# Kernel optimization log

Hardware: AMD Instinct MI355X
Metric: run time of the kernel (lower is better)

Reference implementation:

```python
import jax, jax.numpy as jnp
import numpy as np

B, S, E, H = 2, 2048, 1024, 16
D = E // H  # head_dim = 64


def setup_inputs() -> dict:
    key = jax.random.key(0)
    ks = jax.random.split(key, 6)
    sc = 0.02
    return {
        "hidden_states": jax.random.normal(ks[0], (B, S, E), dtype=jnp.float32),
        "attn_bias": jax.random.normal(ks[1], (S, S), dtype=jnp.float32) * sc,
        "Wqkv": jax.random.normal(ks[2], (E, 3 * E), dtype=jnp.float32) * sc,
        "bqkv": jax.random.normal(ks[3], (3 * E,), dtype=jnp.float32) * sc,
        "Wproj": jax.random.normal(ks[4], (E, E), dtype=jnp.float32) * sc,
        "bproj": jax.random.normal(ks[5], (E,), dtype=jnp.float32) * sc,
    }


def reference(hidden_states, attn_bias, Wqkv, bqkv, Wproj, bproj):
    b, s, e = hidden_states.shape
    qkv = hidden_states @ Wqkv + bqkv                      # [b,s,3e]
    q, k, v = jnp.split(qkv, 3, axis=-1)                   # each [b,s,e]
    cache_key, cache_value = k, v                          # kvCache
    # [b,h,s,d]
    qh = q.reshape(b, s, H, D).transpose(0, 2, 1, 3)
    kh = k.reshape(b, s, H, D).transpose(0, 2, 1, 3)
    vh = v.reshape(b, s, H, D).transpose(0, 2, 1, 3)
    scores = jnp.einsum("bhqd,bhkd->bhqk", qh, kh) / jnp.sqrt(jnp.float32(D))
    scores = scores + attn_bias[:s, :s][None, None]        # learned additive bias
    causal = jnp.tril(jnp.ones((s, s), dtype=bool))
    scores = jnp.where(causal[None, None], scores, jnp.float32(-1e9))
    attn = jax.nn.softmax(scores, axis=-1)
    ctx = jnp.einsum("bhqk,bhkd->bhqd", attn, vh)
    ctx = ctx.transpose(0, 2, 1, 3).reshape(b, s, e)
    out = ctx @ Wproj + bproj                              # resid dropout p=0 -> identity
    return (out, cache_key, cache_value)
```

## Files before the change

### kernel.cpp

```cpp
#include <hip/hip_runtime.h>

#define B_ 2
#define S_ 2048
#define E_ 1024
#define H_ 16
#define D_ 64

typedef short  s16x8 __attribute__((ext_vector_type(8)));
typedef float  f32x4 __attribute__((ext_vector_type(4)));
typedef unsigned short u16x4 __attribute__((ext_vector_type(4)));

__device__ __forceinline__ ushort f2bf(float f) {
    union { float f; unsigned u; } x; x.f = f;
    unsigned u = x.u + 0x7fffu + ((x.u >> 16) & 1u);
    return (ushort)(u >> 16);
}

__global__ __launch_bounds__(256) void cvtx_kernel(
    const float* __restrict__ X, ushort* __restrict__ Xbf)
{
    int i = (blockIdx.x * 256 + threadIdx.x) * 4;
    float4 v = *(const float4*)&X[i];
    u16x4 o;
    o.x = f2bf(v.x); o.y = f2bf(v.y); o.z = f2bf(v.z); o.w = f2bf(v.w);
    *(u16x4*)&Xbf[i] = o;
}

__global__ __launch_bounds__(256) void wtrans_kernel(
    const float* __restrict__ W, ushort* __restrict__ Wt, int Kdim, int Ndim)
{
    __shared__ float tile[64][65];
    int n0 = blockIdx.x * 64, k0 = blockIdx.y * 64;
    int tid = threadIdx.x;
    int c = tid & 63;
#pragma unroll
    for (int r = tid >> 6; r < 64; r += 4)
        tile[r][c] = W[(size_t)(k0 + r) * Ndim + n0 + c];
    __syncthreads();
#pragma unroll
    for (int r = tid >> 6; r < 64; r += 4)
        Wt[(size_t)(n0 + r) * Kdim + k0 + c] = f2bf(tile[c][r]);
}

__global__ __launch_bounds__(256) void gemm_mfma_bt(
    const ushort* __restrict__ A,
    const ushort* __restrict__ Bt,
    const float* __restrict__ bias,
    int M, int N, int K,
    float* __restrict__ C0,
    ushort* __restrict__ Qbf, float* __restrict__ Kf32, ushort* __restrict__ Kbf,
    float* __restrict__ Vf32, int mode)
{
    __shared__ ushort As[128 * 32];
    __shared__ ushort Bs[128 * 32];
    int tid = threadIdx.x;
    int wid = tid >> 6, lane = tid & 63;
    int l15 = lane & 15, quad = lane >> 4;
    int wm = wid >> 1, wn = wid & 1;
    int row0 = blockIdx.y * 128, col0 = blockIdx.x * 128;

    int sr = wid * 16 + (lane >> 2);
    int sk = (lane & 3) * 8;

    f32x4 acc[4][4];
#pragma unroll
    for (int mt = 0; mt < 4; mt++)
#pragma unroll
        for (int nt = 0; nt < 4; nt++) acc[mt][nt] = (f32x4){0.f, 0.f, 0.f, 0.f};

    for (int k0 = 0; k0 < K; k0 += 32) {
        __syncthreads();
#pragma unroll
        for (int c = 0; c < 2; c++) {
            int r = c * 64 + sr;
            __builtin_amdgcn_global_load_lds(
                (const __attribute__((address_space(1))) unsigned int*)
                    &A[(size_t)(row0 + r) * K + k0 + sk],
                (__attribute__((address_space(3))) unsigned int*)&As[r * 32 + sk],
                16, 0, 0);
            __builtin_amdgcn_global_load_lds(
                (const __attribute__((address_space(1))) unsigned int*)
                    &Bt[(size_t)(col0 + r) * K + k0 + sk],
                (__attribute__((address_space(3))) unsigned int*)&Bs[r * 32 + sk],
                16, 0, 0);
        }
        __syncthreads();

        s16x8 af[4], bf[4];
#pragma unroll
        for (int mt = 0; mt < 4; mt++)
            af[mt] = *(const s16x8*)&As[(wm * 64 + mt * 16 + l15) * 32 + quad * 8];
#pragma unroll
        for (int nt = 0; nt < 4; nt++)
            bf[nt] = *(const s16x8*)&Bs[(wn * 64 + nt * 16 + l15) * 32 + quad * 8];
#pragma unroll
        for (int mt = 0; mt < 4; mt++)
#pragma unroll
            for (int nt = 0; nt < 4; nt++)
                acc[mt][nt] = __builtin_amdgcn_mfma_f32_16x16x32_bf16(
                    af[mt], bf[nt], acc[mt][nt], 0, 0, 0);
    }

#pragma unroll
    for (int nt = 0; nt < 4; nt++) {
        int n = col0 + wn * 64 + nt * 16 + l15;
        float bv = bias[n];
        if (mode == 1) {
            int seg = n >> 10;
            int nn = n & (E_ - 1);
#pragma unroll
            for (int mt = 0; mt < 4; mt++)
#pragma unroll
                for (int r = 0; r < 4; r++) {
                    int row = row0 + wm * 64 + mt * 16 + quad * 4 + r;
                    float v = acc[mt][nt][r] + bv;
                    size_t idx = (size_t)row * E_ + nn;
                    if (seg == 0)      Qbf[idx] = f2bf(v);
                    else if (seg == 1) { Kf32[idx] = v; Kbf[idx] = f2bf(v); }
                    else               Vf32[idx] = v;
                }
        } else {
#pragma unroll
            for (int mt = 0; mt < 4; mt++)
#pragma unroll
                for (int r = 0; r < 4; r++) {
                    int row = row0 + wm * 64 + mt * 16 + quad * 4 + r;
                    C0[(size_t)row * N + n] = acc[mt][nt][r] + bv;
                }
        }
    }
}

__global__ __launch_bounds__(256) void vtrans_kernel(
    const float* __restrict__ V, ushort* __restrict__ Vt)
{
    __shared__ float tile[64][65];
    int blk = blockIdx.x;
    int s0 = (blk & 31) * 64;
    int bh = blk >> 5;
    int b = bh >> 4, h = bh & 15;
    int tid = threadIdx.x;
    int d = tid & 63;
#pragma unroll
    for (int i = tid >> 6; i < 64; i += 4)
        tile[i][d] = V[((size_t)(b * S_ + s0 + i)) * E_ + h * 64 + d];
    __syncthreads();
    int lane = tid & 63, w = tid >> 6;
#pragma unroll
    for (int dd = w; dd < 64; dd += 4)
        Vt[((size_t)(bh * 64 + dd)) * S_ + s0 + lane] = f2bf(tile[lane][dd]);
}

__global__ __launch_bounds__(256) void attn_mfma_kernel(
    const ushort* __restrict__ Qbf,
    const ushort* __restrict__ Kbf,
    const ushort* __restrict__ Vt,
    const float* __restrict__ bias,
    ushort* __restrict__ Ctx)
{
    __shared__ ushort Ks[64][72];
    __shared__ ushort Vs[64][72];
    __shared__ ushort Ps[4][16][72];

    int blk = blockIdx.x;
    int bh = blk & 31;
    int pr = blk >> 5;
    int b = bh >> 4, h = bh & 15;
    int tid = threadIdx.x;
    int wid = tid >> 6, lane = tid & 63;
    int l15 = lane & 15, quad = lane >> 4;

    int skey = tid >> 2;
    int scol = (tid & 3) * 16;
    const float scale = 0.125f;

    const size_t krow = (size_t)(b * S_ + skey) * E_ + h * 64 + scol;
    const size_t vrow = (size_t)(bh * 64 + skey) * S_ + scol;

    for (int half = 0; half < 2; half++) {
        int qt = half ? pr : (31 - pr);
        int q0w = qt * 64 + wid * 16;

        const size_t qbase = ((size_t)(b * S_ + q0w + l15)) * E_ + h * 64 + quad * 8;
        s16x8 qa0 = *(const s16x8*)&Qbf[qbase];
        s16x8 qa1 = *(const s16x8*)&Qbf[qbase + 32];

        f32x4 o[4];
#pragma unroll
        for (int dt = 0; dt < 4; dt++) o[dt] = (f32x4){0.f, 0.f, 0.f, 0.f};
        float lsum[4];
#pragma unroll
        for (int r = 0; r < 4; r++) lsum[r] = 0.f;

        float4 kr0 = ((const float4*)&Kbf[krow])[0];
        float4 kr1 = ((const float4*)&Kbf[krow])[1];
        float4 vr0 = ((const float4*)&Vt[vrow])[0];
        float4 vr1 = ((const float4*)&Vt[vrow])[1];
        float bvn[4][4];
#pragma unroll
        for (int r = 0; r < 4; r++)
#pragma unroll
            for (int kt = 0; kt < 4; kt++)
                bvn[r][kt] = bias[(size_t)(q0w + quad * 4 + r) * S_ + kt * 16 + l15];

        for (int t = 0; t <= qt; t++) {
            int j0 = t * 64;
            __syncthreads();
            *(float4*)&Ks[skey][scol]     = kr0;
            *(float4*)&Ks[skey][scol + 8] = kr1;
            *(float4*)&Vs[skey][scol]     = vr0;
            *(float4*)&Vs[skey][scol + 8] = vr1;
            float bv[4][4];
#pragma unroll
            for (int r = 0; r < 4; r++)
#pragma unroll
                for (int kt = 0; kt < 4; kt++) bv[r][kt] = bvn[r][kt];
            __syncthreads();

            if (t < qt) {
                int j1 = j0 + 64;
                kr0 = ((const float4*)&Kbf[krow + (size_t)j1 * E_])[0];
                kr1 = ((const float4*)&Kbf[krow + (size_t)j1 * E_])[1];
                vr0 = ((const float4*)&Vt[vrow + j1])[0];
                vr1 = ((const float4*)&Vt[vrow + j1])[1];
#pragma unroll
                for (int r = 0; r < 4; r++)
#pragma unroll
                    for (int kt = 0; kt < 4; kt++)
                        bvn[r][kt] = bias[(size_t)(q0w + quad * 4 + r) * S_ + j1 + kt * 16 + l15];
            }

            f32x4 s[4];
#pragma unroll
            for (int kt = 0; kt < 4; kt++) {
                s16x8 kb0 = *(const s16x8*)&Ks[kt * 16 + l15][quad * 8];
                s16x8 kb1 = *(const s16x8*)&Ks[kt * 16 + l15][quad * 8 + 32];
                f32x4 acc = (f32x4){0.f, 0.f, 0.f, 0.f};
                acc = __builtin_amdgcn_mfma_f32_16x16x32_bf16(qa0, kb0, acc, 0, 0, 0);
                acc = __builtin_amdgcn_mfma_f32_16x16x32_bf16(qa1, kb1, acc, 0, 0, 0);
                s[kt] = acc;
            }

            bool diag = (t == qt);
#pragma unroll
            for (int r = 0; r < 4; r++) {
                int row = q0w + quad * 4 + r;
#pragma unroll
                for (int kt = 0; kt < 4; kt++) {
                    int j = j0 + kt * 16 + l15;
                    float v = s[kt][r] * scale + bv[r][kt];
                    float p = (diag && j > row) ? 0.f : __expf(v);
                    lsum[r] += p;
                    int chunk = (kt * 2 + (l15 >> 3)) ^ quad;
                    Ps[wid][quad * 4 + r][chunk * 8 + (l15 & 7)] = f2bf(p);
                }
            }

            int cb = (quad ^ (l15 >> 2)) * 8;
            s16x8 pa0 = *(const s16x8*)&Ps[wid][l15][cb];
            s16x8 pa1 = *(const s16x8*)&Ps[wid][l15][cb + 32];
#pragma unroll
            for (int dt = 0; dt < 4; dt++) {
                s16x8 vb0 = *(const s16x8*)&Vs[dt * 16 + l15][quad * 8];
                s16x8 vb1 = *(const s16x8*)&Vs[dt * 16 + l15][quad * 8 + 32];
                o[dt] = __builtin_amdgcn_mfma_f32_16x16x32_bf16(pa0, vb0, o[dt], 0, 0, 0);
                o[dt] = __builtin_amdgcn_mfma_f32_16x16x32_bf16(pa1, vb1, o[dt], 0, 0, 0);
            }
        }

        float inv_l[4];
#pragma unroll
        for (int r = 0; r < 4; r++) {
            float l = lsum[r];
            l += __shfl_xor(l, 1);
            l += __shfl_xor(l, 2);
            l += __shfl_xor(l, 4);
            l += __shfl_xor(l, 8);
            inv_l[r] = 1.f / l;
        }

#pragma unroll
        for (int dt = 0; dt < 4; dt++) {
#pragma unroll
            for (int r = 0; r < 4; r++) {
                int row = q0w + quad * 4 + r;
                Ctx[((size_t)(b * S_ + row)) * E_ + h * 64 + dt * 16 + l15] =
                    f2bf(o[dt][r] * inv_l[r]);
            }
        }
    }
}

extern "C" void kernel_launch(void* const* d_in, const int* in_sizes, int n_in,
                              void* d_out, int out_size, void* d_ws, size_t ws_size,
                              hipStream_t stream) {
    const float* X     = (const float*)d_in[0];
    const float* abias = (const float*)d_in[1];
    const float* Wqkv  = (const float*)d_in[2];
    const float* bqkv  = (const float*)d_in[3];
    const float* Wproj = (const float*)d_in[4];
    const float* bproj = (const float*)d_in[5];

    const size_t plane = (size_t)B_ * S_ * E_;
    float* out  = (float*)d_out;
    float* kout = out + plane;
    float* vout = kout + plane;

    ushort* xbf    = (ushort*)d_ws;
    ushort* qbf    = xbf + plane;
    ushort* kbf    = qbf + plane;
    ushort* vt     = kbf + plane;
    ushort* ctxbf  = xbf;
    ushort* wqkvt  = vt + plane;
    ushort* wprojt = wqkvt + (size_t)3 * E_ * E_;

    const int M = B_ * S_;

    cvtx_kernel<<<dim3(plane / 1024), 256, 0, stream>>>(X, xbf);
    wtrans_kernel<<<dim3(3 * E_ / 64, E_ / 64), 256, 0, stream>>>(Wqkv, wqkvt, E_, 3 * E_);
    wtrans_kernel<<<dim3(E_ / 64, E_ / 64), 256, 0, stream>>>(Wproj, wprojt, E_, E_);

    gemm_mfma_bt<<<dim3(3 * E_ / 128, M / 128), 256, 0, stream>>>(
        xbf, wqkvt, bqkv, M, 3 * E_, E_,
        nullptr, qbf, kout, kbf, vout, 1);

    vtrans_kernel<<<dim3(B_ * H_ * (S_ / 64)), 256, 0, stream>>>(vout, vt);

    attn_mfma_kernel<<<dim3(B_ * H_ * 16), 256, 0, stream>>>(
        qbf, kbf, vt, abias, ctxbf);

    gemm_mfma_bt<<<dim3(E_ / 128, M / 128), 256, 0, stream>>>(
        ctxbf, wprojt, bproj, M, E_, E_,
        out, nullptr, nullptr, nullptr, nullptr, 0);
}
```

Before: 235.2 us.

## Split attention key loop across two wave groups per query slice

Doubles the attention block to 512 threads. Two waves now share each 16-row query slice and handle alternating 64-key tiles, with K/V staged in two LDS buffers. Partial outputs and row sums are combined through shared memory at the end. The goal is more parallelism and latency hiding, since the grid has only 512 blocks. The cost is extra LDS traffic, an extra reduction step and higher register pressure under the 512-thread bound.

Result: slower. 258.0 us (+9.7%).

```diff
diff --git a/kernel.cpp b/kernel.cpp
--- a/kernel.cpp
+++ b/kernel.cpp
@@ -151,16 +151,18 @@
         Vt[((size_t)(bh * 64 + dd)) * S_ + s0 + lane] = f2bf(tile[lane][dd]);
 }
 
-__global__ __launch_bounds__(256) void attn_mfma_kernel(
+__global__ __launch_bounds__(512, 4) void attn_mfma_kernel(
     const ushort* __restrict__ Qbf,
     const ushort* __restrict__ Kbf,
     const ushort* __restrict__ Vt,
     const float* __restrict__ bias,
     ushort* __restrict__ Ctx)
 {
-    __shared__ ushort Ks[64][72];
-    __shared__ ushort Vs[64][72];
-    __shared__ ushort Ps[4][16][72];
+    __shared__ ushort Ks[2][64][72];
+    __shared__ ushort Vs[2][64][72];
+    __shared__ ushort Ps[8][16][72];
+    f32x4 (*Om)[4][64]   = (f32x4(*)[4][64])Ps;
+    float (*Lm)[2][64][4] = (float(*)[2][64][4])Ks;
 
     int blk = blockIdx.x;
     int bh = blk & 31;
@@ -169,9 +171,13 @@
     int tid = threadIdx.x;
     int wid = tid >> 6, lane = tid & 63;
     int l15 = lane & 15, quad = lane >> 4;
-
-    int skey = tid >> 2;
-    int scol = (tid & 3) * 16;
+    int qslice = wid >> 1;
+    int par = wid & 1;
+
+    int ts = tid & 255;
+    int par_s = tid >> 8;
+    int skey = ts >> 2;
+    int scol = (ts & 3) * 16;
     const float scale = 0.125f;
 
     const size_t krow = (size_t)(b * S_ + skey) * E_ + h * 64 + scol;
@@ -179,7 +185,8 @@
 
     for (int half = 0; half < 2; half++) {
         int qt = half ? pr : (31 - pr);
-        int q0w = qt * 64 + wid * 16;
+        int q0w = qt * 64 + qslice * 16;
+        int U = (qt + 2) >> 1;
 
         const size_t qbase = ((size_t)(b * S_ + q0w + l15)) * E_ + h * 64 + quad * 8;
         s16x8 qa0 = *(const s16x8*)&Qbf[qbase];
@@ -192,24 +199,35 @@
 #pragma unroll
         for (int r = 0; r < 4; r++) lsum[r] = 0.f;
 
-        float4 kr0 = ((const float4*)&Kbf[krow])[0];
-        float4 kr1 = ((const float4*)&Kbf[krow])[1];
-        float4 vr0 = ((const float4*)&Vt[vrow])[0];
-        float4 vr1 = ((const float4*)&Vt[vrow])[1];
+        int t0 = (par_s <= qt) ? par_s : qt;
+        size_t koff = krow + (size_t)(t0 * 64) * E_;
+        size_t voff = vrow + (size_t)(t0 * 64);
+        float4 kr0 = ((const float4*)&Kbf[koff])[0];
+        float4 kr1 = ((const float4*)&Kbf[koff])[1];
+        float4 vr0 = ((const float4*)&Vt[voff])[0];
+        float4 vr1 = ((const float4*)&Vt[voff])[1];
+
         float bvn[4][4];
 #pragma unroll
         for (int r = 0; r < 4; r++)
 #pragma unroll
-            for (int kt = 0; kt < 4; kt++)
-                bvn[r][kt] = bias[(size_t)(q0w + quad * 4 + r) * S_ + kt * 16 + l15];
-
-        for (int t = 0; t <= qt; t++) {
-            int j0 = t * 64;
+            for (int kt = 0; kt < 4; kt++) bvn[r][kt] = 0.f;
+        if (par <= qt) {
+#pragma unroll
+            for (int r = 0; r < 4; r++)
+#pragma unroll
+                for (int kt = 0; kt < 4; kt++)
+                    bvn[r][kt] = bias[(size_t)(q0w + quad * 4 + r) * S_
+                                      + par * 64 + kt * 16 + l15];
+        }
+
+        for (int u = 0; u < U; u++) {
+            int tw = 2 * u + par;
             __syncthreads();
-            *(float4*)&Ks[skey][scol]     = kr0;
-            *(float4*)&Ks[skey][scol + 8] = kr1;
-            *(float4*)&Vs[skey][scol]     = vr0;
-            *(float4*)&Vs[skey][scol + 8] = vr1;
+            *(float4*)&Ks[par_s][skey][scol]     = kr0;
+            *(float4*)&Ks[par_s][skey][scol + 8] = kr1;
+            *(float4*)&Vs[par_s][skey][scol]     = vr0;
+            *(float4*)&Vs[par_s][skey][scol + 8] = vr1;
             float bv[4][4];
 #pragma unroll
             for (int r = 0; r < 4; r++)
@@ -217,61 +235,79 @@
                 for (int kt = 0; kt < 4; kt++) bv[r][kt] = bvn[r][kt];
             __syncthreads();
 
-            if (t < qt) {
-                int j1 = j0 + 64;
-                kr0 = ((const float4*)&Kbf[krow + (size_t)j1 * E_])[0];
-                kr1 = ((const float4*)&Kbf[krow + (size_t)j1 * E_])[1];
-                vr0 = ((const float4*)&Vt[vrow + j1])[0];
-                vr1 = ((const float4*)&Vt[vrow + j1])[1];
-#pragma unroll
-                for (int r = 0; r < 4; r++)
-#pragma unroll
-                    for (int kt = 0; kt < 4; kt++)
-                        bvn[r][kt] = bias[(size_t)(q0w + quad * 4 + r) * S_ + j1 + kt * 16 + l15];
+            if (u + 1 < U) {
+                int tn = 2 * (u + 1) + par_s;
+                if (tn > qt) tn = qt;
+                koff = krow + (size_t)(tn * 64) * E_;
+                voff = vrow + (size_t)(tn * 64);
+                kr0 = ((const float4*)&Kbf[koff])[0];
+                kr1 = ((const float4*)&Kbf[koff])[1];
+                vr0 = ((const float4*)&Vt[voff])[0];
+                vr1 = ((const float4*)&Vt[voff])[1];
+                int twn = 2 * (u + 1) + par;
+                if (twn <= qt) {
+#pragma unroll
+                    for (int r = 0; r < 4; r++)
+#pragma unroll
+                        for (int kt = 0; kt < 4; kt++)
+                            bvn[r][kt] = bias[(size_t)(q0w + quad * 4 + r) * S_
+                                              + twn * 64 + kt * 16 + l15];
+                }
             }
 
-            f32x4 s[4];
-#pragma unroll
-            for (int kt = 0; kt < 4; kt++) {
-                s16x8 kb0 = *(const s16x8*)&Ks[kt * 16 + l15][quad * 8];
-                s16x8 kb1 = *(const s16x8*)&Ks[kt * 16 + l15][quad * 8 + 32];
-                f32x4 acc = (f32x4){0.f, 0.f, 0.f, 0.f};
-                acc = __builtin_amdgcn_mfma_f32_16x16x32_bf16(qa0, kb0, acc, 0, 0, 0);
-                acc = __builtin_amdgcn_mfma_f32_16x16x32_bf16(qa1, kb1, acc, 0, 0, 0);
-                s[kt] = acc;
+            if (tw <= qt) {
+                int j0 = tw * 64;
+                f32x4 s[4];
+#pragma unroll
+                for (int kt = 0; kt < 4; kt++) {
+                    s16x8 kb0 = *(const s16x8*)&Ks[par][kt * 16 + l15][quad * 8];
+                    s16x8 kb1 = *(const s16x8*)&Ks[par][kt * 16 + l15][quad * 8 + 32];
+                    f32x4 acc = (f32x4){0.f, 0.f, 0.f, 0.f};
+                    acc = __builtin_amdgcn_mfma_f32_16x16x32_bf16(qa0, kb0, acc, 0, 0, 0);
+                    acc = __builtin_amdgcn_mfma_f32_16x16x32_bf16(qa1, kb1, acc, 0, 0, 0);
+                    s[kt] = acc;
+                }
+
+                bool diag = (tw == qt);
+#pragma unroll
+                for (int r = 0; r < 4; r++) {
+                    int row = q0w + quad * 4 + r;
+#pragma unroll
+                    for (int kt = 0; kt < 4; kt++) {
+                        int j = j0 + kt * 16 + l15;
+                        float v = s[kt][r] * scale + bv[r][kt];
+                        float p = (diag && j > row) ? 0.f : __expf(v);
+                        lsum[r] += p;
+                        int chunk = (kt * 2 + (l15 >> 3)) ^ quad;
+                        Ps[wid][quad * 4 + r][chunk * 8 + (l15 & 7)] = f2bf(p);
+                    }
+                }
+
+                int cb = (quad ^ (l15 >> 2)) * 8;
+                s16x8 pa0 = *(const s16x8*)&Ps[wid][l15][cb];
+                s16x8 pa1 = *(const s16x8*)&Ps[wid][l15][cb + 32];
+#pragma unroll
+                for (int dt = 0; dt < 4; dt++) {
+                    s16x8 vb0 = *(const s16x8*)&Vs[par][dt * 16 + l15][quad * 8];
+                    s16x8 vb1 = *(const s16x8*)&Vs[par][dt * 16 + l15][quad * 8 + 32];
+                    o[dt] = __builtin_amdgcn_mfma_f32_16x16x32_bf16(pa0, vb0, o[dt], 0, 0, 0);
+                    o[dt] = __builtin_amdgcn_mfma_f32_16x16x32_bf16(pa1, vb1, o[dt], 0, 0, 0);
+                }
             }
-
-            bool diag = (t == qt);
-#pragma unroll
-            for (int r = 0; r < 4; r++) {
-                int row = q0w + quad * 4 + r;
-#pragma unroll
-                for (int kt = 0; kt < 4; kt++) {
-                    int j = j0 + kt * 16 + l15;
-                    float v = s[kt][r] * scale + bv[r][kt];
-                    float p = (diag && j > row) ? 0.f : __expf(v);
-                    lsum[r] += p;
-                    int chunk = (kt * 2 + (l15 >> 3)) ^ quad;
-                    Ps[wid][quad * 4 + r][chunk * 8 + (l15 & 7)] = f2bf(p);
-                }
-            }
-
-            int cb = (quad ^ (l15 >> 2)) * 8;
-            s16x8 pa0 = *(const s16x8*)&Ps[wid][l15][cb];
-            s16x8 pa1 = *(const s16x8*)&Ps[wid][l15][cb + 32];
-#pragma unroll
-            for (int dt = 0; dt < 4; dt++) {
-                s16x8 vb0 = *(const s16x8*)&Vs[dt * 16 + l15][quad * 8];
-                s16x8 vb1 = *(const s16x8*)&Vs[dt * 16 + l15][quad * 8 + 32];
-                o[dt] = __builtin_amdgcn_mfma_f32_16x16x32_bf16(pa0, vb0, o[dt], 0, 0, 0);
-                o[dt] = __builtin_amdgcn_mfma_f32_16x16x32_bf16(pa1, vb1, o[dt], 0, 0, 0);
-            }
-        }
+        }
+
+        __syncthreads();
+#pragma unroll
+        for (int dt = 0; dt < 4; dt++)
+            if ((dt >> 1) != par) Om[qslice][dt][lane] = o[dt];
+#pragma unroll
+        for (int r = 0; r < 4; r++) Lm[qslice][par][lane][r] = lsum[r];
+        __syncthreads();
 
         float inv_l[4];
 #pragma unroll
         for (int r = 0; r < 4; r++) {
-            float l = lsum[r];
+            float l = lsum[r] + Lm[qslice][par ^ 1][lane][r];
             l += __shfl_xor(l, 1);
             l += __shfl_xor(l, 2);
             l += __shfl_xor(l, 4);
@@ -281,11 +317,13 @@
 
 #pragma unroll
         for (int dt = 0; dt < 4; dt++) {
+            if ((dt >> 1) != par) continue;
+            f32x4 pv = Om[qslice][dt][lane];
 #pragma unroll
             for (int r = 0; r < 4; r++) {
                 int row = q0w + quad * 4 + r;
                 Ctx[((size_t)(b * S_ + row)) * E_ + h * 64 + dt * 16 + l15] =
-                    f2bf(o[dt][r] * inv_l[r]);
+                    f2bf((o[dt][r] + pv[r]) * inv_l[r]);
             }
         }
     }
@@ -326,7 +364,7 @@
 
     vtrans_kernel<<<dim3(B_ * H_ * (S_ / 64)), 256, 0, stream>>>(vout, vt);
 
-    attn_mfma_kernel<<<dim3(B_ * H_ * 16), 256, 0, stream>>>(
+    attn_mfma_kernel<<<dim3(B_ * H_ * 16), 512, 0, stream>>>(
         qbf, kbf, vt, abias, ctxbf);
 
     gemm_mfma_bt<<<dim3(E_ / 128, M / 128), 256, 0, stream>>>(
```

## Pre-pack causal attention bias into bf16 per-thread tiles and use exp2

Applied to the files above, without the earlier changes.

Adds a prep kernel that packs the lower-triangular 64x64 tiles of the attention bias into bf16, pre-scaled by log2(e) and laid out so each thread loads its 16 values with two contiguous 16-byte reads. The attention kernel then does one vector load per tile instead of 16 scattered fp32 loads, and uses a raw v_exp_f32 (exp2) with the scale folded into one fma. The block-to-(batch,head) mapping is also reordered so blocks of the same head are adjacent. This costs an extra kernel launch, reuses the Wqkv workspace region, and rounds the bias to bf16 precision.

Result: no change. 237.2 us (+0.9%).

```diff
diff --git a/kernel.cpp b/kernel.cpp
--- a/kernel.cpp
+++ b/kernel.cpp
@@ -16,6 +16,10 @@
     return (ushort)(u >> 16);
 }
 
+__device__ __forceinline__ float fast_exp2(float x) {
+    float r; asm("v_exp_f32 %0, %1" : "=v"(r) : "v"(x)); return r;
+}
+
 __global__ __launch_bounds__(256) void cvtx_kernel(
     const float* __restrict__ X, ushort* __restrict__ Xbf)
 {
@@ -40,6 +44,33 @@
 #pragma unroll
     for (int r = tid >> 6; r < 64; r += 4)
         Wt[(size_t)(n0 + r) * Kdim + k0 + c] = f2bf(tile[c][r]);
+}
+
+__global__ __launch_bounds__(256) void prep_bias_kernel(
+    const float* __restrict__ bias, ushort* __restrict__ biasT)
+{
+    int L = blockIdx.x;
+    int qi = (int)((sqrtf(8.0f * (float)L + 1.0f) - 1.0f) * 0.5f);
+    while ((qi + 1) * (qi + 2) / 2 <= L) qi++;
+    while (qi * (qi + 1) / 2 > L) qi--;
+    int ki = L - qi * (qi + 1) / 2;
+    int tid = threadIdx.x;
+    int w = tid >> 6, quad = (tid >> 4) & 3, l15 = tid & 15;
+    const float LOG2E = 1.4426950408889634f;
+    s16x8 h0 = (s16x8){0,0,0,0,0,0,0,0}, h1 = (s16x8){0,0,0,0,0,0,0,0};
+#pragma unroll
+    for (int r = 0; r < 4; r++)
+#pragma unroll
+        for (int kt = 0; kt < 4; kt++) {
+            float v = bias[(size_t)(qi * 64 + w * 16 + quad * 4 + r) * S_
+                           + ki * 64 + kt * 16 + l15] * LOG2E;
+            ushort u = f2bf(v);
+            int idx = r * 4 + kt;
+            if (idx < 8) h0[idx] = (short)u; else h1[idx - 8] = (short)u;
+        }
+    ushort* dst = &biasT[((size_t)L * 256 + tid) * 16];
+    *(s16x8*)dst = h0;
+    *(s16x8*)(dst + 8) = h1;
 }
 
 __global__ __launch_bounds__(256) void gemm_mfma_bt(
@@ -155,7 +186,7 @@
     const ushort* __restrict__ Qbf,
     const ushort* __restrict__ Kbf,
     const ushort* __restrict__ Vt,
-    const float* __restrict__ bias,
+    const ushort* __restrict__ biasT,
     ushort* __restrict__ Ctx)
 {
     __shared__ ushort Ks[64][72];
@@ -163,8 +194,8 @@
     __shared__ ushort Ps[4][16][72];
 
     int blk = blockIdx.x;
-    int bh = blk & 31;
-    int pr = blk >> 5;
+    int bh = blk >> 4;
+    int pr = blk & 15;
     int b = bh >> 4, h = bh & 15;
     int tid = threadIdx.x;
     int wid = tid >> 6, lane = tid & 63;
@@ -172,7 +203,7 @@
 
     int skey = tid >> 2;
     int scol = (tid & 3) * 16;
-    const float scale = 0.125f;
+    const float scale_l2e = 0.18033688011112042f;
 
     const size_t krow = (size_t)(b * S_ + skey) * E_ + h * 64 + scol;
     const size_t vrow = (size_t)(bh * 64 + skey) * S_ + scol;
@@ -196,12 +227,9 @@
         float4 kr1 = ((const float4*)&Kbf[krow])[1];
         float4 vr0 = ((const float4*)&Vt[vrow])[0];
         float4 vr1 = ((const float4*)&Vt[vrow])[1];
-        float bvn[4][4];
-#pragma unroll
-        for (int r = 0; r < 4; r++)
-#pragma unroll
-            for (int kt = 0; kt < 4; kt++)
-                bvn[r][kt] = bias[(size_t)(q0w + quad * 4 + r) * S_ + kt * 16 + l15];
+        const ushort* bt = &biasT[((size_t)(qt * (qt + 1) / 2) * 256 + tid) * 16];
+        s16x8 bn0 = *(const s16x8*)bt;
+        s16x8 bn1 = *(const s16x8*)(bt + 8);
 
         for (int t = 0; t <= qt; t++) {
             int j0 = t * 64;
@@ -210,11 +238,7 @@
             *(float4*)&Ks[skey][scol + 8] = kr1;
             *(float4*)&Vs[skey][scol]     = vr0;
             *(float4*)&Vs[skey][scol + 8] = vr1;
-            float bv[4][4];
-#pragma unroll
-            for (int r = 0; r < 4; r++)
-#pragma unroll
-                for (int kt = 0; kt < 4; kt++) bv[r][kt] = bvn[r][kt];
+            s16x8 b0 = bn0, b1 = bn1;
             __syncthreads();
 
             if (t < qt) {
@@ -223,11 +247,9 @@
                 kr1 = ((const float4*)&Kbf[krow + (size_t)j1 * E_])[1];
                 vr0 = ((const float4*)&Vt[vrow + j1])[0];
                 vr1 = ((const float4*)&Vt[vrow + j1])[1];
-#pragma unroll
-                for (int r = 0; r < 4; r++)
-#pragma unroll
-                    for (int kt = 0; kt < 4; kt++)
-                        bvn[r][kt] = bias[(size_t)(q0w + quad * 4 + r) * S_ + j1 + kt * 16 + l15];
+                const ushort* btn = bt + (size_t)(t + 1) * 4096;
+                bn0 = *(const s16x8*)btn;
+                bn1 = *(const s16x8*)(btn + 8);
             }
 
             f32x4 s[4];
@@ -248,8 +270,11 @@
 #pragma unroll
                 for (int kt = 0; kt < 4; kt++) {
                     int j = j0 + kt * 16 + l15;
-                    float v = s[kt][r] * scale + bv[r][kt];
-                    float p = (diag && j > row) ? 0.f : __expf(v);
+                    int idx = r * 4 + kt;
+                    ushort ub = (ushort)((idx < 8) ? b0[idx] : b1[idx - 8]);
+                    union { unsigned u; float f; } bc; bc.u = ((unsigned)ub) << 16;
+                    float v = fmaf(s[kt][r], scale_l2e, bc.f);
+                    float p = (diag && j > row) ? 0.f : fast_exp2(v);
                     lsum[r] += p;
                     int chunk = (kt * 2 + (l15 >> 3)) ^ quad;
                     Ps[wid][quad * 4 + r][chunk * 8 + (l15 & 7)] = f2bf(p);
@@ -313,6 +338,7 @@
     ushort* ctxbf  = xbf;
     ushort* wqkvt  = vt + plane;
     ushort* wprojt = wqkvt + (size_t)3 * E_ * E_;
+    ushort* biasT  = wqkvt;
 
     const int M = B_ * S_;
 
@@ -326,8 +352,10 @@
 
     vtrans_kernel<<<dim3(B_ * H_ * (S_ / 64)), 256, 0, stream>>>(vout, vt);
 
+    prep_bias_kernel<<<dim3(528), 256, 0, stream>>>(abias, biasT);
+
     attn_mfma_kernel<<<dim3(B_ * H_ * 16), 256, 0, stream>>>(
-        qbf, kbf, vt, abias, ctxbf);
+        qbf, kbf, vt, biasT, ctxbf);
 
     gemm_mfma_bt<<<dim3(E_ / 128, M / 128), 256, 0, stream>>>(
         ctxbf, wprojt, bproj, M, E_, E_,
```
